# Kernel tuning notes

Measured on AMD Instinct MI355X. Metric: run time of the kernel, lower is better.

Reference implementation:

```python
import jax, jax.numpy as jnp
import numpy as np

BATCH = 8192
FEATURES = 8192
INITIAL_SPARSITY_RATE = 0.5


def setup_inputs() -> dict:
    key = jax.random.key(0)
    k1, _ = jax.random.split(key)
    inputs = jax.random.normal(k1, (BATCH, FEATURES), dtype=jnp.float32)
    # trainable scalar weight, shape (1,), constant-initialized
    sparsity_rate = jnp.full((1,), INITIAL_SPARSITY_RATE, dtype=jnp.float32)
    return {"inputs": inputs, "sparsity_rate": sparsity_rate}


def reference(inputs, sparsity_rate):
    # inputs: [B, F]; sparsity_rate: [1]
    n = inputs.shape[-1]
    # descending sort along feature axis
    sorted_desc = -jnp.sort(-inputs, axis=-1)
    # per-call threshold index (integer cast, non-differentiable like TF's tf.cast)
    rate = jnp.clip(sparsity_rate[0], 0.0, 1.0)
    idx = jax.lax.stop_gradient((rate * jnp.float32(n)).astype(jnp.int32))
    thresh = jnp.take(sorted_desc, idx, axis=-1)           # [B]: value at rank `idx`
    max_in = jnp.max(inputs, axis=-1)                      # [B]
    t_r = max_in - thresh                                  # [B]
    # relu-masked weights: relu(x + t_r - max) == relu(x - thresh)
    w_t = jax.nn.relu(inputs + t_r[:, None] - max_in[:, None])
    weighted_exp = w_t * jnp.exp(inputs)                   # [B, F]
    sum_we = jnp.sum(weighted_exp, axis=-1, keepdims=True)
    return weighted_exp / sum_we
```

## Files before the change

kernel.cpp:

```cpp
#include <hip/hip_runtime.h>

#define ROWS 8192
#define COLS 8192
#define TPB  256
#define EPT  32
#define VPT  8

__device__ __forceinline__ unsigned f2k(float x) {
    unsigned u = __float_as_uint(x);
    return (u & 0x80000000u) ? ~u : (u | 0x80000000u);
}
__device__ __forceinline__ float k2f(unsigned k) {
    unsigned u = (k & 0x80000000u) ? (k & 0x7FFFFFFFu) : ~k;
    return __uint_as_float(u);
}

__global__ __launch_bounds__(TPB, 4)
void rsoftmax_kernel(const float* __restrict__ in,
                     const float* __restrict__ rate_p,
                     float* __restrict__ out)
{
    const int t   = threadIdx.x;
    const int row = blockIdx.x;
    const float4* in4  = (const float4*)(in  + (size_t)row * COLS);
    float4*       out4 = (float4*)      (out + (size_t)row * COLS);

    unsigned key[EPT];
    #pragma unroll
    for (int j = 0; j < VPT; ++j) {
        float4 v = in4[t + j * TPB];
        key[4*j+0] = f2k(v.x);
        key[4*j+1] = f2k(v.y);
        key[4*j+2] = f2k(v.z);
        key[4*j+3] = f2k(v.w);
    }

    float rate = rate_p[0];
    rate = fminf(fmaxf(rate, 0.0f), 1.0f);
    int idx = (int)(rate * (float)COLS);
    if (idx > COLS - 1) idx = COLS - 1;
    if (idx < 0) idx = 0;

    __shared__ unsigned sHist[256];
    __shared__ unsigned sScan[256];
    __shared__ unsigned sK, sPfx;
    __shared__ float    sW[4];
    __shared__ float    sInv;

    if (t == 0) { sK = (unsigned)(idx + 1); sPfx = 0u; }
    __syncthreads();

    #pragma unroll
    for (int pass = 0; pass < 4; ++pass) {
        const int      s      = 24 - 8 * pass;
        const unsigned himask = (pass == 0) ? 0u : (0xFFFFFFFFu << (s + 8));

        sHist[t] = 0u;
        __syncthreads();
        const unsigned pfx = sPfx;
        const unsigned kk  = sK;

        #pragma unroll
        for (int j = 0; j < EPT; ++j) {
            if (((key[j] ^ pfx) & himask) == 0u)
                atomicAdd(&sHist[(key[j] >> s) & 0xFFu], 1u);
        }
        __syncthreads();

        sScan[t] = sHist[t];
        __syncthreads();
        #pragma unroll
        for (int off = 1; off < 256; off <<= 1) {
            unsigned v = (t + off < 256) ? sScan[t + off] : 0u;
            __syncthreads();
            sScan[t] += v;
            __syncthreads();
        }

        unsigned st = sScan[t];
        unsigned sn = (t == 255) ? 0u : sScan[t + 1];
        if (st >= kk && sn < kk) {
            sPfx = pfx | ((unsigned)t << s);
            sK   = kk - sn;
        }
        __syncthreads();
    }

    const float thr = k2f(sPfx);

    float lsum = 0.0f;
    #pragma unroll
    for (int j = 0; j < EPT; ++j) {
        float x = k2f(key[j]);
        float w = fmaxf(x - thr, 0.0f);
        lsum += w * __expf(x);
    }
    #pragma unroll
    for (int off = 32; off > 0; off >>= 1)
        lsum += __shfl_down(lsum, off, 64);
    if ((t & 63) == 0) sW[t >> 6] = lsum;
    __syncthreads();
    if (t == 0) sInv = 1.0f / (sW[0] + sW[1] + sW[2] + sW[3]);
    __syncthreads();
    const float inv = sInv;

    #pragma unroll
    for (int j = 0; j < VPT; ++j) {
        float4 o;
        float x0 = k2f(key[4*j+0]); o.x = fmaxf(x0 - thr, 0.0f) * __expf(x0) * inv;
        float x1 = k2f(key[4*j+1]); o.y = fmaxf(x1 - thr, 0.0f) * __expf(x1) * inv;
        float x2 = k2f(key[4*j+2]); o.z = fmaxf(x2 - thr, 0.0f) * __expf(x2) * inv;
        float x3 = k2f(key[4*j+3]); o.w = fmaxf(x3 - thr, 0.0f) * __expf(x3) * inv;
        out4[t + j * TPB] = o;
    }
}

extern "C" void kernel_launch(void* const* d_in, const int* in_sizes, int n_in,
                              void* d_out, int out_size, void* d_ws, size_t ws_size,
                              hipStream_t stream)
{
    const float* in   = (const float*)d_in[0];
    const float* rate = (const float*)d_in[1];
    float*       out  = (float*)d_out;
    rsoftmax_kernel<<<dim3(ROWS), dim3(TPB), 0, stream>>>(in, rate, out);
}
```

Measured before the change: 461.6 us.

## Use per-wave histograms and wave-shuffle scan in radix select

Replaces the single shared histogram with per-wave histograms, which cuts atomic contention. The 256-entry block scan built from shared memory and many barriers becomes a wave-level shuffle suffix scan plus a small cross-wave combine, which removes most __syncthreads per pass. It also caches the weighted exponentials in registers so exp is not computed twice. The cost is extra shared memory and about 32 more live registers, which may lower occupancy.

```diff
diff --git a/kernel.cpp b/kernel.cpp
--- a/kernel.cpp
+++ b/kernel.cpp
@@ -5,6 +5,7 @@
 #define TPB  256
 #define EPT  32
 #define VPT  8
+#define NW   4
 
 __device__ __forceinline__ unsigned f2k(float x) {
     unsigned u = __float_as_uint(x);
@@ -20,8 +21,10 @@
                      const float* __restrict__ rate_p,
                      float* __restrict__ out)
 {
-    const int t   = threadIdx.x;
-    const int row = blockIdx.x;
+    const int t    = threadIdx.x;
+    const int lane = t & 63;
+    const int wave = t >> 6;
+    const int row  = blockIdx.x;
     const float4* in4  = (const float4*)(in  + (size_t)row * COLS);
     float4*       out4 = (float4*)      (out + (size_t)row * COLS);
 
@@ -41,76 +44,84 @@
     if (idx > COLS - 1) idx = COLS - 1;
     if (idx < 0) idx = 0;
 
-    __shared__ unsigned sHist[256];
-    __shared__ unsigned sScan[256];
+    __shared__ unsigned sHistW[NW][256];
+    __shared__ unsigned sWaveTot[NW];
     __shared__ unsigned sK, sPfx;
-    __shared__ float    sW[4];
+    __shared__ float    sSum[NW];
     __shared__ float    sInv;
 
     if (t == 0) { sK = (unsigned)(idx + 1); sPfx = 0u; }
-    __syncthreads();
 
     #pragma unroll
     for (int pass = 0; pass < 4; ++pass) {
         const int      s      = 24 - 8 * pass;
         const unsigned himask = (pass == 0) ? 0u : (0xFFFFFFFFu << (s + 8));
 
-        sHist[t] = 0u;
         __syncthreads();
         const unsigned pfx = sPfx;
         const unsigned kk  = sK;
 
         #pragma unroll
+        for (int i = 0; i < 4; ++i) sHistW[wave][lane + 64*i] = 0u;
+
+        #pragma unroll
         for (int j = 0; j < EPT; ++j) {
             if (((key[j] ^ pfx) & himask) == 0u)
-                atomicAdd(&sHist[(key[j] >> s) & 0xFFu], 1u);
+                atomicAdd(&sHistW[wave][(key[j] >> s) & 0xFFu], 1u);
         }
         __syncthreads();
 
-        sScan[t] = sHist[t];
+        const unsigned h = sHistW[0][t] + sHistW[1][t] + sHistW[2][t] + sHistW[3][t];
+
+        unsigned v = h;
+        #pragma unroll
+        for (int off = 1; off < 64; off <<= 1) {
+            unsigned u = __shfl_down(v, off, 64);
+            v += (lane + off < 64) ? u : 0u;
+        }
+        if (lane == 0) sWaveTot[wave] = v;
         __syncthreads();
+
+        unsigned above = 0u;
         #pragma unroll
-        for (int off = 1; off < 256; off <<= 1) {
-            unsigned v = (t + off < 256) ? sScan[t + off] : 0u;
-            __syncthreads();
-            sScan[t] += v;
-            __syncthreads();
-        }
+        for (int w = 0; w < NW; ++w)
+            if (w > wave) above += sWaveTot[w];
 
-        unsigned st = sScan[t];
-        unsigned sn = (t == 255) ? 0u : sScan[t + 1];
+        const unsigned st = v + above;
+        const unsigned sn = st - h;
         if (st >= kk && sn < kk) {
             sPfx = pfx | ((unsigned)t << s);
             sK   = kk - sn;
         }
-        __syncthreads();
     }
-
+    __syncthreads();
     const float thr = k2f(sPfx);
 
+    float wx[EPT];
     float lsum = 0.0f;
     #pragma unroll
     for (int j = 0; j < EPT; ++j) {
         float x = k2f(key[j]);
-        float w = fmaxf(x - thr, 0.0f);
-        lsum += w * __expf(x);
+        float e = fmaxf(x - thr, 0.0f) * __expf(x);
+        wx[j] = e;
+        lsum += e;
     }
     #pragma unroll
     for (int off = 32; off > 0; off >>= 1)
         lsum += __shfl_down(lsum, off, 64);
-    if ((t & 63) == 0) sW[t >> 6] = lsum;
+    if (lane == 0) sSum[wave] = lsum;
     __syncthreads();
-    if (t == 0) sInv = 1.0f / (sW[0] + sW[1] + sW[2] + sW[3]);
+    if (t == 0) sInv = 1.0f / (sSum[0] + sSum[1] + sSum[2] + sSum[3]);
     __syncthreads();
     const float inv = sInv;
 
     #pragma unroll
     for (int j = 0; j < VPT; ++j) {
         float4 o;
-        float x0 = k2f(key[4*j+0]); o.x = fmaxf(x0 - thr, 0.0f) * __expf(x0) * inv;
-        float x1 = k2f(key[4*j+1]); o.y = fmaxf(x1 - thr, 0.0f) * __expf(x1) * inv;
-        float x2 = k2f(key[4*j+2]); o.z = fmaxf(x2 - thr, 0.0f) * __expf(x2) * inv;
-        float x3 = k2f(key[4*j+3]); o.w = fmaxf(x3 - thr, 0.0f) * __expf(x3) * inv;
+        o.x = wx[4*j+0] * inv;
+        o.y = wx[4*j+1] * inv;
+        o.z = wx[4*j+2] * inv;
+        o.w = wx[4*j+3] * inv;
         out4[t + j * TPB] = o;
     }
 }
```

Result: no change. 457.4 us (-0.9%).
